# Kernel optimization log

Measured on AMD Instinct MI355X. Metric: run time of the kernel, lower is better.

## Reference

```python
import jax, jax.numpy as jnp
import numpy as np

B, L, D, NH, NITEMS = 256, 200, 128, 2, 100000
HD = D // NH
LAMB = 0.6
NEG = -1e9

_PARAM_SHAPES = dict(
    item_emb=(NITEMS, D), pos_emb=(L, D),
    W_ei=(D, D), b_ei=(D,), W_eo=(D, D), b_eo=(D,), b_iah=(D,), b_oah=(D,),
    w_ih=(3 * D, 2 * D), b_ih=(3 * D,), w_hh=(3 * D, D), b_hh=(3 * D,),
    ln1_g=(D,), ln1_b=(D,),
    Wq=(D, D), bq=(D,), Wk=(D, D), bk=(D,), Wv=(D, D), bv=(D,), Wo=(D, D), bo=(D,),
    ln2_g=(D,), ln2_b=(D,), W1=(D, D), b1=(D,), W2=(D, D), b2=(D,),
    lnf_g=(D,), lnf_b=(D,),
)


def setup_inputs() -> dict:
    key = jax.random.key(0)
    ks = jax.random.split(key, len(_PARAM_SHAPES) + 2)
    stdv = 1.0 / np.sqrt(D)  # GCSAN._init_weights: uniform(-stdv, stdv) on ALL params
    p = {}
    for i, (name, shp) in enumerate(_PARAM_SHAPES.items()):
        p[name] = jax.random.uniform(ks[i], shp, jnp.float32, -stdv, stdv)
    lens = jax.random.randint(ks[-2], (B,), L // 4, L + 1)
    vals = jax.random.randint(ks[-1], (B, L), 1, NITEMS)
    # trailing zero padding, as the original break-on-zero loop assumes
    seqs = jnp.where(jnp.arange(L)[None, :] < lens[:, None], vals, 0).astype(jnp.int32)
    p['seqs'] = seqs
    p['lens'] = lens.astype(jnp.int32)
    return p


def _ln(x, g, b):
    mu = x.mean(-1, keepdims=True)
    var = ((x - mu) ** 2).mean(-1, keepdims=True)
    return (x - mu) / jnp.sqrt(var + 1e-5) * g + b


def _build_graph(seqs):
    # Vectorized replacement of _get_slice (per-row np.unique + adjacency build)
    def per_row(seq):
        s = jnp.sort(seq)
        first = jnp.concatenate([jnp.ones((1,), bool), s[1:] != s[:-1]])
        pos = jnp.cumsum(first) - 1  # compaction target of each first-occurrence
        items = jnp.zeros((L,), seq.dtype).at[jnp.where(first, pos, L)].set(s, mode='drop')
        n_u = first.sum()
        search = jnp.where(jnp.arange(L) < n_u, items, jnp.iinfo(jnp.int32).max)
        alias = jnp.searchsorted(search, seq).astype(jnp.int32)
        return items, alias
    items, alias = jax.vmap(per_row)(seqs)
    valid = seqs[:, 1:] > 0  # edge (i -> i+1) exists until first pad
    u = jnp.where(valid, alias[:, :-1], L)  # route masked edges to dummy row L
    v = jnp.where(valid, alias[:, 1:], L)
    bidx = jnp.arange(B)[:, None]
    uA = jnp.zeros((B, L + 1, L + 1), jnp.float32).at[bidx, u, v].set(1.0)[:, :L, :L]
    in_deg = jnp.maximum(uA.sum(1), 1.0)
    out_deg = jnp.maximum(uA.sum(2), 1.0)
    A_in = jnp.swapaxes(uA, 1, 2) / in_deg[:, :, None]   # A[i,j] = uA[j,i]/in_deg[i]
    A_out = uA / out_deg[:, :, None]                     # A[i,k] = uA[i,k]/out_deg[i]
    return alias, jnp.concatenate([A_in, A_out], axis=2), items  # A: [B, L, 2L]


def reference(item_emb, pos_emb, W_ei, b_ei, W_eo, b_eo, b_iah, b_oah,
              w_ih, b_ih, w_hh, b_hh, ln1_g, ln1_b, Wq, bq, Wk, bk, Wv, bv,
              Wo, bo, ln2_g, ln2_b, W1, b1, W2, b2, lnf_g, lnf_b, seqs, lens):
    alias, A, items = _build_graph(seqs)
    hidden = item_emb[items]  # [B, L, D]
    # SR-GNN gated cell, step = n_layers = 1
    for _ in range(1):
        h_in = jnp.einsum('bij,bjd->bid', A[:, :, :L], hidden @ W_ei.T + b_ei) + b_iah
        h_out = jnp.einsum('bij,bjd->bid', A[:, :, L:], hidden @ W_eo.T + b_eo) + b_oah
        gi = jnp.concatenate([h_in, h_out], -1) @ w_ih.T + b_ih
        gh = hidden @ w_hh.T + b_hh
        i_r, i_i, i_n = jnp.split(gi, 3, -1)
        h_r, h_i, h_n = jnp.split(gh, 3, -1)
        r = jax.nn.sigmoid(i_r + h_r)
        z = jax.nn.sigmoid(i_i + h_i)
        ng = jnp.tanh(i_n + r * h_n)
        hidden = ng + z * (hidden - ng)
    bidx = jnp.arange(B)
    seq_hidden = hidden[bidx[:, None], alias]  # alias-gather back to sequence order
    last_idx = lens - 1
    ht = seq_hidden[bidx, last_idx]
    x = seq_hidden + pos_emb[None, :, :]
    tl_mask = (seqs > 0)[:, :, None].astype(x.dtype)
    x = x * tl_mask
    causal = jnp.triu(jnp.ones((L, L), bool), 1)  # True = masked future (bidirectional=False)
    # SASRec-style block: ln -> MHA residual -> ln -> pointwise FFN residual
    q_in = _ln(x, ln1_g, ln1_b)
    heads = lambda t: t.reshape(B, L, NH, HD).transpose(0, 2, 1, 3)
    q = heads(q_in @ Wq.T + bq)
    k = heads(x @ Wk.T + bk)
    v = heads(x @ Wv.T + bv)
    sc = jnp.einsum('bhqd,bhkd->bhqk', q, k) / jnp.sqrt(jnp.asarray(HD, x.dtype))
    sc = jnp.where(causal[None, None], NEG, sc)
    attn = jax.nn.softmax(sc, -1)
    mo = jnp.einsum('bhqk,bhkd->bhqd', attn, v).transpose(0, 2, 1, 3).reshape(B, L, D) @ Wo.T + bo
    x = q_in + mo
    h = _ln(x, ln2_g, ln2_b)
    x = h + jax.nn.relu(h @ W1.T + b1) @ W2.T + b2
    x = x * tl_mask
    log_feats = _ln(x, lnf_g, lnf_b)
    out = log_feats[bidx, last_idx]
    return LAMB * out + (1.0 - LAMB) * ht
```

## Files before the change

kernel.cpp:

```cpp
#include <hip/hip_runtime.h>
#include <hip/hip_bf16.h>

#define Bb 256
#define Ll 200
#define Dd 128
#define BL (Bb*Ll)

typedef __hip_bfloat16 bf16;
typedef __attribute__((ext_vector_type(8))) short short8;
typedef __attribute__((ext_vector_type(4))) unsigned short ushort4v;
typedef __attribute__((ext_vector_type(4))) float floatx4;

__device__ __forceinline__ float b2f(bf16 v) { return __bfloat162float(v); }
__device__ __forceinline__ bf16  f2b(float v) { return __float2bfloat16(v); }
__device__ __forceinline__ float us2f(unsigned short u) { return __uint_as_float(((unsigned)u) << 16); }
__device__ __forceinline__ unsigned short f2us(float v) { bf16 t = f2b(v); return *(unsigned short*)&t; }
__device__ __forceinline__ float ldf(const void* p, int i, int f32) {
  return f32 ? ((const float*)p)[i] : b2f(((const bf16*)p)[i]);
}
__device__ __forceinline__ int detect_f32(const unsigned short* __restrict__ w) {
  unsigned short u = w[threadIdx.x & 63];
  return (__ballot(((u >> 7) & 0xFF) >= 0x7F) != 0ull) ? 1 : 0;
}
__device__ __forceinline__ void load_lds16(const void* g, void* l) {
  __builtin_amdgcn_global_load_lds((const __attribute__((address_space(1))) unsigned int*)g,
                                   (__attribute__((address_space(3))) unsigned int*)l, 16, 0, 0);
}
__device__ __forceinline__ short8 emb_chunk8(const void* __restrict__ emb, int it, int g, int f32) {
  short8 o;
  if (f32) {
    const float4* e = (const float4*)((const float*)emb + (size_t)it * 128 + g * 8);
    float4 a = e[0], b = e[1];
    o[0] = (short)f2us(a.x); o[1] = (short)f2us(a.y); o[2] = (short)f2us(a.z); o[3] = (short)f2us(a.w);
    o[4] = (short)f2us(b.x); o[5] = (short)f2us(b.y); o[6] = (short)f2us(b.z); o[7] = (short)f2us(b.w);
  } else {
    o = ((const short8*)((const bf16*)emb + (size_t)it * 128))[g];
  }
  return o;
}

struct PackP {
  const void *W_ei,*W_eo,*w_ih,*w_hh,*Wk,*Wv,*Wqp,*Wop,*W1p,*W2p,*pos;
  const void *b_ei,*b_eo,*b_ih,*b_hh,*bk,*bv,*bqp,*bop,*b1p,*b2p,*biah,*boah;
  const void *ln1g,*ln1b,*ln2g,*ln2b,*lnfg,*lnfb;
  bf16 *cWhe,*cWih,*cWhh,*cWkv,*cWq,*cWo,*cW1,*cW2,*cPos;
  float *bias_he,*bias_gi,*bias_gh,*bias_kv,*cbq,*cbo,*cb1,*cb2,*cbiah,*cboah,*cln;
  const int* seqs;
  int *alias_g, *items_g; float *rin_g, *rout_g; unsigned *adj_g, *adjT_g;
};
__global__ __launch_bounds__(256) void k01(PackP p) {
  __shared__ alignas(16) int s[Ll];
  __shared__ int al[Ll], its[Ll];
  __shared__ alignas(4) unsigned char isf[Ll];
  __shared__ unsigned adjL[Ll*8], adjTL[Ll*8];
  if (blockIdx.x >= Bb) {
    int idx = (blockIdx.x - Bb) * 256 + threadIdx.x;
    int f32 = detect_f32((const unsigned short*)p.W_ei);
    if (idx < 131072) {
      if (idx < 32768) {
        int r = idx >> 7, c = idx & 127;
        p.cWhe[idx] = f2b(r < 128 ? ldf(p.W_ei, r*128+c, f32) : ldf(p.W_eo, (r-128)*128+c, f32));
      } else p.cWih[idx-32768] = f2b(ldf(p.w_ih, idx-32768, f32));
    } else if (idx < 278528) {
      if (idx < 180224)      p.cWhh[idx-131072] = f2b(ldf(p.w_hh, idx-131072, f32));
      else if (idx < 212992) {
        int i = idx - 180224; int r = i >> 7, c = i & 127;
        p.cWkv[i] = f2b(r < 128 ? ldf(p.Wk, r*128+c, f32) : ldf(p.Wv, (r-128)*128+c, f32));
      }
      else if (idx < 229376) p.cWq[idx-212992] = f2b(ldf(p.Wqp, idx-212992, f32));
      else if (idx < 245760) p.cWo[idx-229376] = f2b(ldf(p.Wop, idx-229376, f32));
      else if (idx < 262144) p.cW1[idx-245760] = f2b(ldf(p.W1p, idx-245760, f32));
      else                   p.cW2[idx-262144] = f2b(ldf(p.W2p, idx-262144, f32));
    } else if (idx < 304128) {
      p.cPos[idx-278528] = f2b(ldf(p.pos, idx-278528, f32));
    } else {
      int j = idx - 304128;
      if      (j < 256)  p.bias_he[j]     = (j<128) ? ldf(p.b_ei,j,f32) : ldf(p.b_eo,j-128,f32);
      else if (j < 640)  p.bias_gi[j-256] = ldf(p.b_ih, j-256, f32);
      else if (j < 1024) p.bias_gh[j-640] = ldf(p.b_hh, j-640, f32);
      else if (j < 1280) { int c=j-1024; p.bias_kv[c] = (c<128)? ldf(p.bk,c,f32): ldf(p.bv,c-128,f32); }
      else if (j < 1408) p.cbq[j-1280]   = ldf(p.bqp, j-1280, f32);
      else if (j < 1536) p.cbo[j-1408]   = ldf(p.bop, j-1408, f32);
      else if (j < 1664) p.cb1[j-1536]   = ldf(p.b1p, j-1536, f32);
      else if (j < 1792) p.cb2[j-1664]   = ldf(p.b2p, j-1664, f32);
      else if (j < 1920) p.cbiah[j-1792] = ldf(p.biah, j-1792, f32);
      else if (j < 2048) p.cboah[j-1920] = ldf(p.boah, j-1920, f32);
      else {
        int i = j - 2048, g = i >> 7, c2 = i & 127;
        const void* s6 = g==0?p.ln1g: g==1?p.ln1b: g==2?p.ln2g: g==3?p.ln2b: g==4?p.lnfg: p.lnfb;
        p.cln[i] = ldf(s6, c2, f32);
      }
    }
    return;
  }
  int b = blockIdx.x, t = threadIdx.x;
  if (t < Ll) s[t] = p.seqs[b*Ll + t];
  for (int i = t; i < Ll*8; i += 256) { adjL[i] = 0u; adjTL[i] = 0u; }
  __syncthreads();
  const int4* s4 = (const int4*)s;
  if (t < Ll) {
    int v = s[t]; int dup = 0;
    int nb = t >> 2;
    for (int j4 = 0; j4 < nb; j4++) {
      int4 sv = s4[j4];
      dup |= (sv.x==v) | (sv.y==v) | (sv.z==v) | (sv.w==v);
    }
    for (int j = nb*4; j < t; j++) dup |= (s[j]==v);
    isf[t] = dup ? 0 : 1; its[t] = 0;
  }
  __syncthreads();
  const unsigned* isfw = (const unsigned*)isf;
  if (t < Ll) {
    int v = s[t], r = 0;
    for (int j4 = 0; j4 < Ll/4; j4++) {
      int4 sv = s4[j4];
      unsigned fw = isfw[j4];
      r += ((fw & 0xffu)       && sv.x < v);
      r += ((fw & 0xff00u)     && sv.y < v);
      r += ((fw & 0xff0000u)   && sv.z < v);
      r += ((fw & 0xff000000u) && sv.w < v);
    }
    al[t] = r;
  }
  __syncthreads();
  if (t < Ll && isf[t]) its[al[t]] = s[t];
  if (t < Ll-1 && s[t+1] > 0) {
    int u = al[t], v = al[t+1];
    atomicOr(&adjL [u*8 + (v >> 5)], 1u << (v & 31));
    atomicOr(&adjTL[v*8 + (u >> 5)], 1u << (u & 31));
  }
  __syncthreads();
  if (t < Ll) {
    int od = 0, id = 0;
    for (int wd = 0; wd < 7; wd++) { od += __popc(adjL[t*8+wd]); id += __popc(adjTL[t*8+wd]); }
    p.rout_g [b*Ll + t] = 1.0f / (float)max(od, 1);
    p.rin_g  [b*Ll + t] = 1.0f / (float)max(id, 1);
    p.alias_g[b*Ll + t] = al[t];
    p.items_g[b*Ll + t] = its[t];
  }
  for (int i = t; i < Ll*8; i += 256) { p.adj_g[b*Ll*8 + i] = adjL[i]; p.adjT_g[b*Ll*8 + i] = adjTL[i]; }
}

__global__ __launch_bounds__(256) void gemm_he2(const void* __restrict__ emb, const int* __restrict__ items_g,
    const bf16* __restrict__ W, const float* __restrict__ bias,
    bf16* __restrict__ out_lo, int Nlo, bf16* __restrict__ out_hi, int Nhi, int split)
{
  __shared__ short As[128*128];
  __shared__ short Ws[128*128];
  int t = threadIdx.x;
  int wave = t >> 6, lane = t & 63;
  int q = lane >> 4, mr = lane & 15;
  int wm = wave & 1, wn = wave >> 1;
  int m0 = blockIdx.x * 128;
  int f32 = detect_f32((const unsigned short*)emb);
  {
    int r = t >> 1, half = t & 1;
    int it = items_g[m0 + r];
#pragma unroll
    for (int g8 = 0; g8 < 8; g8++) {
      int g = half*8 + g8;
      short8 o = emb_chunk8(emb, it, g, f32);
      *(short8*)&As[r*128 + (g ^ (r & 15))*8] = o;
    }
  }
  int srow = lane >> 4, c16 = lane & 15;
  for (int nt = 0; nt < 5; nt++) {
    int n0 = nt * 128;
#pragma unroll
    for (int i = 0; i < 8; i++) {
      int seg = wave*8 + i;
      int r = seg*4 + srow;
      int gch = c16 ^ (r & 15);
      load_lds16(W + (size_t)(n0 + r) * 128 + gch*8, &Ws[seg*512]);
    }
    __syncthreads();
    floatx4 acc[4][4] = {};
#pragma unroll
    for (int kk = 0; kk < 4; kk++) {
      short8 af[4], wf[4];
#pragma unroll
      for (int i = 0; i < 4; i++) {
        int row = wm*64 + i*16 + mr;
        af[i] = *(const short8*)(&As[row*128 + ((kk*4+q) ^ (row&15))*8]);
      }
#pragma unroll
      for (int j = 0; j < 4; j++) {
        int row = wn*64 + j*16 + mr;
        wf[j] = *(const short8*)(&Ws[row*128 + ((kk*4+q) ^ (row&15))*8]);
      }
#pragma unroll
      for (int i = 0; i < 4; i++)
#pragma unroll
        for (int j = 0; j < 4; j++)
          acc[i][j] = __builtin_amdgcn_mfma_f32_16x16x32_bf16(wf[j], af[i], acc[i][j], 0, 0, 0);
    }
#pragma unroll
    for (int j = 0; j < 4; j++) {
      int ng = n0 + wn*64 + j*16 + q*4;
      floatx4 bs = *(const floatx4*)(bias + ng);
      bf16* outp; int col, stride;
      if (ng < split) { outp = out_lo; col = ng; stride = Nlo; }
      else            { outp = out_hi; col = ng - split; stride = Nhi; }
#pragma unroll
      for (int i = 0; i < 4; i++) {
        int m = m0 + wm*64 + i*16 + mr;
        ushort4v o;
#pragma unroll
        for (int e = 0; e < 4; e++) o[e] = f2us(acc[i][j][e] + bs[e]);
        *(ushort4v*)(outp + (size_t)m * stride + col) = o;
      }
    }
    if (nt + 1 < 5) __syncthreads();
  }
}

template<int K>
__global__ __launch_bounds__(256) void gemm6(const bf16* __restrict__ A, const bf16* __restrict__ W,
    const float* __restrict__ bias,
    bf16* __restrict__ out_lo, int Nlo, bf16* __restrict__ out_hi, int Nhi, int split)
{
  __shared__ short As[128*128];
  __shared__ short Ws[128*128];
  int t = threadIdx.x;
  int wave = t >> 6, lane = t & 63;
  int q = lane >> 4, mr = lane & 15;
  int wm = wave & 1, wn = wave >> 1;
  int m0 = blockIdx.x * 128, n0 = blockIdx.y * 128;
  int srow = lane >> 4;
  int c16 = lane & 15;
  floatx4 acc[4][4] = {};
  for (int k0 = 0; k0 < K; k0 += 128) {
#pragma unroll
    for (int i = 0; i < 8; i++) {
      int seg = wave*8 + i;
      int r = seg*4 + srow;
      int gch = c16 ^ (r & 15);
      load_lds16(A + (size_t)(m0 + r) * K + k0 + gch*8, &As[seg*512]);
      load_lds16(W + (size_t)(n0 + r) * K + k0 + gch*8, &Ws[seg*512]);
    }
    __syncthreads();
#pragma unroll
    for (int kk = 0; kk < 4; kk++) {
      short8 af[4], wf[4];
#pragma unroll
      for (int i = 0; i < 4; i++) {
        int row = wm*64 + i*16 + mr;
        af[i] = *(const short8*)(&As[row*128 + ((kk*4+q) ^ (row&15))*8]);
      }
#pragma unroll
      for (int j = 0; j < 4; j++) {
        int row = wn*64 + j*16 + mr;
        wf[j] = *(const short8*)(&Ws[row*128 + ((kk*4+q) ^ (row&15))*8]);
      }
#pragma unroll
      for (int i = 0; i < 4; i++)
#pragma unroll
        for (int j = 0; j < 4; j++)
          acc[i][j] = __builtin_amdgcn_mfma_f32_16x16x32_bf16(wf[j], af[i], acc[i][j], 0, 0, 0);
    }
    if (k0 + 128 < K) __syncthreads();
  }
#pragma unroll
  for (int j = 0; j < 4; j++) {
    int ng = n0 + wn*64 + j*16 + q*4;
    floatx4 bs = *(const floatx4*)(bias + ng);
    bf16* outp; int col, stride;
    if (ng < split) { outp = out_lo; col = ng; stride = Nlo; }
    else            { outp = out_hi; col = ng - split; stride = Nhi; }
#pragma unroll
    for (int i = 0; i < 4; i++) {
      int m = m0 + wm*64 + i*16 + mr;
      ushort4v o;
#pragma unroll
      for (int e = 0; e < 4; e++) o[e] = f2us(acc[i][j][e] + bs[e]);
      *(ushort4v*)(outp + (size_t)m * stride + col) = o;
    }
  }
}

__global__ __launch_bounds__(256) void k3_agg(const bf16* __restrict__ he,
    const unsigned* __restrict__ adj_g, const unsigned* __restrict__ adjT_g,
    const float* __restrict__ rin_g, const float* __restrict__ rout_g,
    const float* __restrict__ cbiah, const float* __restrict__ cboah, bf16* __restrict__ hio)
{
  int b = blockIdx.x / 25, chunk = blockIdx.x % 25;
  int wave = threadIdx.x >> 6, lane = threadIdx.x & 63;
  bool isIn = lane < 32;
  int c = isIn ? 4*lane : 128 + 4*(lane-32);
  const bf16* heb = he + (size_t)b * Ll * 256;
  bf16* hiob = hio + (size_t)b * Ll * 256;
  float bias0 = isIn ? cbiah[c]   : cboah[c-128];
  float bias1 = isIn ? cbiah[c+1] : cboah[c-127];
  float bias2 = isIn ? cbiah[c+2] : cboah[c-126];
  float bias3 = isIn ? cbiah[c+3] : cboah[c-125];
#pragma unroll
  for (int s = 0; s < 2; s++) {
    int i = chunk*8 + wave + 4*s;
    const unsigned* mrow = (isIn ? adjT_g : adj_g) + ((size_t)b*Ll + i) * 8;
    float a0=0.f, a1=0.f, a2=0.f, a3=0.f;
    for (int wd = 0; wd < 7; wd++) {
      unsigned bits = mrow[wd];
      while (bits) {
        int j = (wd << 5) + __builtin_ctz(bits); bits &= bits - 1;
        ushort4v h4 = *(const ushort4v*)(heb + (size_t)j*256 + c);
        a0 += us2f(h4.x); a1 += us2f(h4.y); a2 += us2f(h4.z); a3 += us2f(h4.w);
      }
    }
    float r = isIn ? rin_g[b*Ll + i] : rout_g[b*Ll + i];
    ushort4v o;
    o.x = f2us(bias0 + r*a0); o.y = f2us(bias1 + r*a1);
    o.z = f2us(bias2 + r*a2); o.w = f2us(bias3 + r*a3);
    *(ushort4v*)(hiob + (size_t)i*256 + c) = o;
  }
}

__global__ __launch_bounds__(256) void kv_fused(const bf16* __restrict__ gi, const bf16* __restrict__ gh,
    const void* __restrict__ emb, const int* __restrict__ seqs,
    const int* __restrict__ alias_g, const int* __restrict__ lens,
    const bf16* __restrict__ cPos, const bf16* __restrict__ cWkv, const float* __restrict__ bias_kv,
    bf16* __restrict__ kv, float* __restrict__ ht)
{
  __shared__ short xs[208*136];
  __shared__ int aliasL[Ll], seqL[Ll];
  int b = blockIdx.x, t = threadIdx.x;
  int wave = t >> 6, lane = t & 63, q = lane >> 4, mr = lane & 15;
  int li = lens[b] - 1;
  int f32 = detect_f32((const unsigned short*)emb);
  if (t < Ll) { aliasL[t] = alias_g[b*Ll + t]; seqL[t] = seqs[b*Ll + t]; }
  for (int u = t; u < 8*136; u += 256) xs[Ll*136 + u] = 0;
  __syncthreads();
  for (int u = t; u < Ll*16; u += 256) {
    int tpos = u >> 4, jv = u & 15;
    int a = aliasL[tpos];
    int it = seqL[tpos];
    const short8* gin = (const short8*)(gi + ((size_t)b*Ll + a) * 384);
    const short8* ghn = (const short8*)(gh + ((size_t)b*Ll + a) * 384);
    short8 vir = gin[jv], vii = gin[16+jv], vnn = gin[32+jv];
    short8 whr = ghn[jv], whi = ghn[16+jv], whn = ghn[32+jv];
    short8 hv  = emb_chunk8(emb, it, jv, f32);
    short8 pv  = ((const short8*)(cPos + tpos * Dd))[jv];
    bool isLast = (tpos == li);
    short8 o;
#pragma unroll
    for (int e = 0; e < 8; e++) {
      float ir = us2f((unsigned short)vir[e]), ii = us2f((unsigned short)vii[e]), inn = us2f((unsigned short)vnn[e]);
      float hr = us2f((unsigned short)whr[e]), hi = us2f((unsigned short)whi[e]), hn = us2f((unsigned short)whn[e]);
      float r  = 1.f / (1.f + __expf(-(ir + hr)));
      float z  = 1.f / (1.f + __expf(-(ii + hi)));
      float arg = inn + r * hn;
      float ex = __expf(-2.f * arg);
      float ng = (1.f - ex) / (1.f + ex);
      float h  = us2f((unsigned short)hv[e]);
      float sh = ng + z * (h - ng);
      o[e] = (short)f2us(sh + us2f((unsigned short)pv[e]));
      if (isLast) ht[b*Dd + jv*8 + e] = sh;
    }
    *(short8*)&xs[tpos*136 + jv*8] = o;
  }
  __syncthreads();
  short8 wf[4][4];
#pragma unroll
  for (int kk = 0; kk < 4; kk++)
#pragma unroll
    for (int j = 0; j < 4; j++) {
      int n = wave*64 + j*16 + mr;
      wf[kk][j] = *(const short8*)(cWkv + (size_t)n*128 + kk*32 + q*8);
    }
  for (int mt = 0; mt < 13; mt++) {
    short8 af[4];
#pragma unroll
    for (int kk = 0; kk < 4; kk++)
      af[kk] = *(const short8*)&xs[(mt*16 + mr)*136 + (kk*4+q)*8];
    floatx4 acc[4] = {};
#pragma unroll
    for (int kk = 0; kk < 4; kk++)
#pragma unroll
      for (int j = 0; j < 4; j++)
        acc[j] = __builtin_amdgcn_mfma_f32_16x16x32_bf16(wf[kk][j], af[kk], acc[j], 0, 0, 0);
    int m = mt*16 + mr;
    if (m < Ll) {
#pragma unroll
      for (int j = 0; j < 4; j++) {
        int n = wave*64 + j*16 + q*4;
        floatx4 bs = *(const floatx4*)(bias_kv + n);
        ushort4v o;
#pragma unroll
        for (int e = 0; e < 4; e++) o[e] = f2us(acc[j][e] + bs[e]);
        *(ushort4v*)(kv + ((size_t)b*Ll + m)*256 + n) = o;
      }
    }
  }
}

struct FinalP {
  const bf16 *kv; const float* ht; const bf16* cPos;
  const bf16 *cWq, *cWo, *cW1, *cW2;
  const float *cbq, *cbo, *cb1, *cb2, *cln;
  const int* lens; const void* wei;
  void* out;
};
__device__ __forceinline__ float dot128i(const bf16* __restrict__ wrow, const float* __restrict__ vin) {
  const short8* wr = (const short8*)wrow;
  float a0=0.f, a1=0.f, a2=0.f, a3=0.f;
#pragma unroll
  for (int kk = 0; kk < 4; kk++) {
    short8 w0 = wr[kk*4+0], w1 = wr[kk*4+1], w2 = wr[kk*4+2], w3 = wr[kk*4+3];
#pragma unroll
    for (int j = 0; j < 8; j++) {
      a0 += vin[kk*32 +      j] * us2f((unsigned short)w0[j]);
      a1 += vin[kk*32 + 8  + j] * us2f((unsigned short)w1[j]);
      a2 += vin[kk*32 + 16 + j] * us2f((unsigned short)w2[j]);
      a3 += vin[kk*32 + 24 + j] * us2f((unsigned short)w3[j]);
    }
  }
  return (a0+a1)+(a2+a3);
}
__device__ __forceinline__ float wave_sum(float v) {
#pragma unroll
  for (int m = 1; m < 64; m <<= 1) v += __shfl_xor(v, m, 64);
  return v;
}
__device__ __forceinline__ float wave_max(float v) {
#pragma unroll
  for (int m = 1; m < 64; m <<= 1) v = fmaxf(v, __shfl_xor(v, m, 64));
  return v;
}
__global__ __launch_bounds__(256) void k7_final(FinalP p)
{
  __shared__ float sred[8];
  __shared__ float qin[128], qv[128], aout[128], hh[128], f1[128];
  __shared__ float pb0[256], pb1[256];
  __shared__ floatx4 av4[8][32];
  int b = blockIdx.x, t = threadIdx.x, c = t;
  int w = t >> 6, ln = t & 63;
  int li = p.lens[b] - 1;
  int f32 = detect_f32((const unsigned short*)p.wei);
  float xv = (c < 128) ? (p.ht[b*Dd + c] + b2f(p.cPos[li*Dd + c])) : 0.f;
  float s = wave_sum(xv), s2 = wave_sum(xv*xv);
  if (ln == 0) { sred[w] = s; sred[4+w] = s2; }
  __syncthreads();
  float mu = (sred[0]+sred[1]+sred[2]+sred[3]) * (1.f/128.f);
  float ms = (sred[4]+sred[5]+sred[6]+sred[7]) * (1.f/128.f);
  float rs = rsqrtf(fmaxf(ms - mu*mu, 0.f) + 1e-5f);
  __syncthreads();
  if (c < 128) qin[c] = (xv - mu) * rs * p.cln[c] + p.cln[128+c];
  __syncthreads();
  if (c < 128) qv[c] = p.cbq[c] + dot128i(p.cWq + c*128, qin);
  __syncthreads();
  const bf16* kvb = p.kv + (size_t)b * Ll * 256;
  float s0 = -3.0e38f, s1 = -3.0e38f;
  if (t <= li) {
    const short8* kr = (const short8*)(kvb + (size_t)t*256);
    float a00=0.f,a01=0.f,a10=0.f,a11=0.f;
#pragma unroll
    for (int kk = 0; kk < 4; kk++) {
      short8 k0 = kr[kk*2], k1 = kr[kk*2+1], k2 = kr[8+kk*2], k3 = kr[8+kk*2+1];
#pragma unroll
      for (int j = 0; j < 8; j++) {
        a00 += qv[kk*16 + j]      * us2f((unsigned short)k0[j]);
        a01 += qv[kk*16 + 8 + j]  * us2f((unsigned short)k1[j]);
        a10 += qv[64 + kk*16 + j]     * us2f((unsigned short)k2[j]);
        a11 += qv[64 + kk*16 + 8 + j] * us2f((unsigned short)k3[j]);
      }
    }
    s0 = (a00+a01) * 0.125f; s1 = (a10+a11) * 0.125f;
  }
  float m0 = wave_max(s0), m1 = wave_max(s1);
  if (ln == 0) { sred[w] = m0; sred[4+w] = m1; }
  __syncthreads();
  m0 = fmaxf(fmaxf(sred[0],sred[1]), fmaxf(sred[2],sred[3]));
  m1 = fmaxf(fmaxf(sred[4],sred[5]), fmaxf(sred[6],sred[7]));
  __syncthreads();
  float e0 = (t <= li) ? __expf(s0 - m0) : 0.f;
  float e1 = (t <= li) ? __expf(s1 - m1) : 0.f;
  pb0[t] = e0; pb1[t] = e1;
  float l0 = wave_sum(e0), l1 = wave_sum(e1);
  if (ln == 0) { sred[w] = l0; sred[4+w] = l1; }
  __syncthreads();
  l0 = sred[0]+sred[1]+sred[2]+sred[3];
  l1 = sred[4]+sred[5]+sred[6]+sred[7];
  {
    int part = t >> 5, cq = t & 31, ch = cq * 4;
    int cnt = li + 1, cpp = (cnt + 7) >> 3;
    int j0 = part * cpp, j1 = min(j0 + cpp, cnt);
    const float* pbh = (ch < 64) ? pb0 : pb1;
    float a0=0.f,a1=0.f,a2=0.f,a3=0.f;
#pragma unroll 4
    for (int j = j0; j < j1; j++) {
      ushort4v v4 = *(const ushort4v*)(kvb + (size_t)j*256 + 128 + ch);
      float pw = pbh[j];
      a0 += pw*us2f(v4.x); a1 += pw*us2f(v4.y); a2 += pw*us2f(v4.z); a3 += pw*us2f(v4.w);
    }
    floatx4 o = {a0,a1,a2,a3};
    av4[part][cq] = o;
  }
  __syncthreads();
  if (c < 128) {
    float l = (c < 64) ? l0 : l1;
    float acc = 0.f;
#pragma unroll
    for (int pp = 0; pp < 8; pp++) acc += ((const float*)&av4[pp][c>>2])[c&3];
    aout[c] = acc / l;
  }
  __syncthreads();
  float x2v = 0.f;
  if (c < 128) x2v = qin[c] + p.cbo[c] + dot128i(p.cWo + c*128, aout);
  s = wave_sum((c<128)?x2v:0.f); s2 = wave_sum((c<128)?x2v*x2v:0.f);
  if (ln == 0) { sred[w] = s; sred[4+w] = s2; }
  __syncthreads();
  mu = (sred[0]+sred[1]+sred[2]+sred[3]) * (1.f/128.f);
  ms = (sred[4]+sred[5]+sred[6]+sred[7]) * (1.f/128.f);
  rs = rsqrtf(fmaxf(ms - mu*mu, 0.f) + 1e-5f);
  __syncthreads();
  if (c < 128) hh[c] = (x2v - mu) * rs * p.cln[256+c] + p.cln[384+c];
  __syncthreads();
  if (c < 128) f1[c] = fmaxf(p.cb1[c] + dot128i(p.cW1 + c*128, hh), 0.f);
  __syncthreads();
  float x3v = 0.f;
  if (c < 128) x3v = hh[c] + p.cb2[c] + dot128i(p.cW2 + c*128, f1);
  s = wave_sum((c<128)?x3v:0.f); s2 = wave_sum((c<128)?x3v*x3v:0.f);
  if (ln == 0) { sred[w] = s; sred[4+w] = s2; }
  __syncthreads();
  mu = (sred[0]+sred[1]+sred[2]+sred[3]) * (1.f/128.f);
  ms = (sred[4]+sred[5]+sred[6]+sred[7]) * (1.f/128.f);
  rs = rsqrtf(fmaxf(ms - mu*mu, 0.f) + 1e-5f);
  if (c < 128) {
    float lf = (x3v - mu) * rs * p.cln[512+c] + p.cln[640+c];
    float outv = 0.6f * lf + 0.4f * p.ht[b*Dd + c];
    if (f32) ((float*)p.out)[b*Dd + c] = outv;
    else     ((bf16*)p.out)[b*Dd + c]  = f2b(outv);
  }
}

extern "C" void kernel_launch(void* const* d_in, const int* in_sizes, int n_in,
                              void* d_out, int out_size, void* d_ws, size_t ws_size,
                              hipStream_t stream)
{
  (void)in_sizes; (void)n_in; (void)out_size; (void)ws_size;
  const void* item_emb = d_in[0];
  const int* seqs = (const int*)d_in[30];
  const int* lens = (const int*)d_in[31];

  char* wsp = (char*)d_ws;
  size_t o = 0;
  auto alloc = [&](size_t sz) { void* p = wsp + o; o += (sz + 255) & ~(size_t)255; return p; };
  int*      alias_g = (int*)alloc((size_t)BL*4);
  int*      items_g = (int*)alloc((size_t)BL*4);
  float*    rin_g   = (float*)alloc((size_t)BL*4);
  float*    rout_g  = (float*)alloc((size_t)BL*4);
  unsigned* adj_g   = (unsigned*)alloc((size_t)BL*8*4);
  unsigned* adjT_g  = (unsigned*)alloc((size_t)BL*8*4);
  float*    ht_g    = (float*)alloc((size_t)Bb*Dd*4);
  bf16*     cWhe    = (bf16*)alloc(32768*2);
  bf16*     cWhh    = (bf16*)alloc(49152*2);
  bf16*     cWih    = (bf16*)alloc(98304*2);
  bf16*     cWkv    = (bf16*)alloc(32768*2);
  bf16*     cWq     = (bf16*)alloc(16384*2);
  bf16*     cWo     = (bf16*)alloc(16384*2);
  bf16*     cW1     = (bf16*)alloc(16384*2);
  bf16*     cW2     = (bf16*)alloc(16384*2);
  bf16*     cPos    = (bf16*)alloc(25600*2);
  float*    bias_he = (float*)alloc(256*4);
  float*    bias_gh = (float*)alloc(384*4);
  float*    bias_gi = (float*)alloc(384*4);
  float*    bias_kv = (float*)alloc(256*4);
  float*    cbq     = (float*)alloc(128*4);
  float*    cbo     = (float*)alloc(128*4);
  float*    cb1     = (float*)alloc(128*4);
  float*    cb2     = (float*)alloc(128*4);
  float*    cbiah   = (float*)alloc(128*4);
  float*    cboah   = (float*)alloc(128*4);
  float*    cln     = (float*)alloc(768*4);
  bf16*     he      = (bf16*)alloc((size_t)BL*256*2);
  bf16*     hio     = (bf16*)alloc((size_t)BL*256*2);
  bf16*     gi      = (bf16*)alloc((size_t)BL*384*2);
  bf16*     gh      = (bf16*)alloc((size_t)BL*384*2);
  bf16*     kv = hio;

  PackP pp = { d_in[2], d_in[4], d_in[8], d_in[10], d_in[16], d_in[18], d_in[14], d_in[20],
               d_in[24], d_in[26], d_in[1],
               d_in[3], d_in[5], d_in[9], d_in[11], d_in[17], d_in[19], d_in[15], d_in[21],
               d_in[25], d_in[27], d_in[6], d_in[7],
               d_in[12], d_in[13], d_in[22], d_in[23], d_in[28], d_in[29],
               cWhe, cWih, cWhh, cWkv, cWq, cWo, cW1, cW2, cPos,
               bias_he, bias_gi, bias_gh, bias_kv, cbq, cbo, cb1, cb2, cbiah, cboah, cln,
               seqs, alias_g, items_g, rin_g, rout_g, adj_g, adjT_g };
  k01<<<Bb + 1199, 256, 0, stream>>>(pp);
  gemm_he2<<<BL/128, 256, 0, stream>>>(item_emb, items_g, cWhe, bias_he, he, 256, gh, 384, 256);
  k3_agg<<<Bb*25, 256, 0, stream>>>(he, adj_g, adjT_g, rin_g, rout_g, cbiah, cboah, hio);
  gemm6<256><<<dim3(BL/128, 3), 256, 0, stream>>>(hio, cWih, bias_gi, gi, 384, gi, 384, 1<<30);
  kv_fused<<<Bb, 256, 0, stream>>>(gi, gh, item_emb, seqs, alias_g, lens, cPos, cWkv, bias_kv, kv, ht_g);
  FinalP fp = { kv, ht_g, cPos, cWq, cWo, cW1, cW2, cbq, cbo, cb1, cb2, cln, lens, d_in[2], d_out };
  k7_final<<<Bb, 256, 0, stream>>>(fp);
}
```

Baseline: 273.5 us.

## Fuse K/V projection with final attention kernel, keep KV in LDS

Merges the kv_fused and k7_final kernels into one per-batch kernel that writes the K/V projection and the last-position hidden state into shared memory. The attention, FFN and layer norms then read them from there. This removes a kernel launch and the global round trip of the per-batch KV buffer (about 100 KB per batch) and of ht. In exchange the kernel allocates about 160 KB of LDS in one shared pool that is reused between stages, which limits occupancy to one block per CU. It also keeps the 256 blocks of 256 threads, so most of the GPU stays lightly loaded.

```diff
diff --git a/kernel.cpp b/kernel.cpp
--- a/kernel.cpp
+++ b/kernel.cpp
@@ -314,31 +314,74 @@
   }
 }
 
-__global__ __launch_bounds__(256) void kv_fused(const bf16* __restrict__ gi, const bf16* __restrict__ gh,
-    const void* __restrict__ emb, const int* __restrict__ seqs,
-    const int* __restrict__ alias_g, const int* __restrict__ lens,
-    const bf16* __restrict__ cPos, const bf16* __restrict__ cWkv, const float* __restrict__ bias_kv,
-    bf16* __restrict__ kv, float* __restrict__ ht)
+struct KAP {
+  const bf16 *gi, *gh; const void* emb; const int* seqs; const int* alias_g; const int* lens;
+  const bf16 *cPos, *cWkv; const float* bias_kv;
+  const bf16 *cWq, *cWo, *cW1, *cW2;
+  const float *cbq, *cbo, *cb1, *cb2, *cln;
+  void* out;
+};
+__device__ __forceinline__ float dot128i(const bf16* __restrict__ wrow, const float* __restrict__ vin) {
+  const short8* wr = (const short8*)wrow;
+  float a0=0.f, a1=0.f, a2=0.f, a3=0.f;
+#pragma unroll
+  for (int kk = 0; kk < 4; kk++) {
+    short8 w0 = wr[kk*4+0], w1 = wr[kk*4+1], w2 = wr[kk*4+2], w3 = wr[kk*4+3];
+#pragma unroll
+    for (int j = 0; j < 8; j++) {
+      a0 += vin[kk*32 +      j] * us2f((unsigned short)w0[j]);
+      a1 += vin[kk*32 + 8  + j] * us2f((unsigned short)w1[j]);
+      a2 += vin[kk*32 + 16 + j] * us2f((unsigned short)w2[j]);
+      a3 += vin[kk*32 + 24 + j] * us2f((unsigned short)w3[j]);
+    }
+  }
+  return (a0+a1)+(a2+a3);
+}
+__device__ __forceinline__ float wave_sum(float v) {
+#pragma unroll
+  for (int m = 1; m < 64; m <<= 1) v += __shfl_xor(v, m, 64);
+  return v;
+}
+__device__ __forceinline__ float wave_max(float v) {
+#pragma unroll
+  for (int m = 1; m < 64; m <<= 1) v = fmaxf(v, __shfl_xor(v, m, 64));
+  return v;
+}
+__global__ __launch_bounds__(256) void kv_attn(KAP p)
 {
-  __shared__ short xs[208*136];
-  __shared__ int aliasL[Ll], seqL[Ll];
+  __shared__ __align__(16) char pool[162688];
+  short* xs   = (short*)pool;
+  short* kvL  = (short*)(pool + 56576);
+  float* htL  = (float*)(pool + 56576 + 105600);
+  int* aliasL = (int*)(pool + 56576);
+  int* seqL   = aliasL + 200;
+  float* qin  = (float*)pool;
+  float* qv   = qin + 128;
+  float* aout = qv + 128;
+  float* hh   = aout + 128;
+  float* f1   = hh + 128;
+  float* pb0  = f1 + 128;
+  float* pb1  = pb0 + 256;
+  floatx4* av4 = (floatx4*)(pb1 + 256);
+  float* sred = (float*)(av4 + 8*32);
+
   int b = blockIdx.x, t = threadIdx.x;
   int wave = t >> 6, lane = t & 63, q = lane >> 4, mr = lane & 15;
-  int li = lens[b] - 1;
-  int f32 = detect_f32((const unsigned short*)emb);
-  if (t < Ll) { aliasL[t] = alias_g[b*Ll + t]; seqL[t] = seqs[b*Ll + t]; }
+  int li = p.lens[b] - 1;
+  int f32 = detect_f32((const unsigned short*)p.emb);
+  if (t < Ll) { aliasL[t] = p.alias_g[b*Ll + t]; seqL[t] = p.seqs[b*Ll + t]; }
   for (int u = t; u < 8*136; u += 256) xs[Ll*136 + u] = 0;
   __syncthreads();
   for (int u = t; u < Ll*16; u += 256) {
     int tpos = u >> 4, jv = u & 15;
     int a = aliasL[tpos];
     int it = seqL[tpos];
-    const short8* gin = (const short8*)(gi + ((size_t)b*Ll + a) * 384);
-    const short8* ghn = (const short8*)(gh + ((size_t)b*Ll + a) * 384);
+    const short8* gin = (const short8*)(p.gi + ((size_t)b*Ll + a) * 384);
+    const short8* ghn = (const short8*)(p.gh + ((size_t)b*Ll + a) * 384);
     short8 vir = gin[jv], vii = gin[16+jv], vnn = gin[32+jv];
     short8 whr = ghn[jv], whi = ghn[16+jv], whn = ghn[32+jv];
-    short8 hv  = emb_chunk8(emb, it, jv, f32);
-    short8 pv  = ((const short8*)(cPos + tpos * Dd))[jv];
+    short8 hv  = emb_chunk8(p.emb, it, jv, f32);
+    short8 pv  = ((const short8*)(p.cPos + tpos * Dd))[jv];
     bool isLast = (tpos == li);
     short8 o;
 #pragma unroll
@@ -353,89 +396,48 @@
       float h  = us2f((unsigned short)hv[e]);
       float sh = ng + z * (h - ng);
       o[e] = (short)f2us(sh + us2f((unsigned short)pv[e]));
-      if (isLast) ht[b*Dd + jv*8 + e] = sh;
+      if (isLast) htL[jv*8 + e] = sh;
     }
     *(short8*)&xs[tpos*136 + jv*8] = o;
   }
   __syncthreads();
-  short8 wf[4][4];
-#pragma unroll
-  for (int kk = 0; kk < 4; kk++)
-#pragma unroll
-    for (int j = 0; j < 4; j++) {
-      int n = wave*64 + j*16 + mr;
-      wf[kk][j] = *(const short8*)(cWkv + (size_t)n*128 + kk*32 + q*8);
-    }
-  for (int mt = 0; mt < 13; mt++) {
-    short8 af[4];
+  {
+    short8 wf[4][4];
 #pragma unroll
     for (int kk = 0; kk < 4; kk++)
-      af[kk] = *(const short8*)&xs[(mt*16 + mr)*136 + (kk*4+q)*8];
-    floatx4 acc[4] = {};
-#pragma unroll
-    for (int kk = 0; kk < 4; kk++)
-#pragma unroll
-      for (int j = 0; j < 4; j++)
-        acc[j] = __builtin_amdgcn_mfma_f32_16x16x32_bf16(wf[kk][j], af[kk], acc[j], 0, 0, 0);
-    int m = mt*16 + mr;
-    if (m < Ll) {
 #pragma unroll
       for (int j = 0; j < 4; j++) {
-        int n = wave*64 + j*16 + q*4;
-        floatx4 bs = *(const floatx4*)(bias_kv + n);
-        ushort4v o;
-#pragma unroll
-        for (int e = 0; e < 4; e++) o[e] = f2us(acc[j][e] + bs[e]);
-        *(ushort4v*)(kv + ((size_t)b*Ll + m)*256 + n) = o;
-      }
-    }
-  }
-}
-
-struct FinalP {
-  const bf16 *kv; const float* ht; const bf16* cPos;
-  const bf16 *cWq, *cWo, *cW1, *cW2;
-  const float *cbq, *cbo, *cb1, *cb2, *cln;
-  const int* lens; const void* wei;
-  void* out;
-};
-__device__ __forceinline__ float dot128i(const bf16* __restrict__ wrow, const float* __restrict__ vin) {
-  const short8* wr = (const short8*)wrow;
-  float a0=0.f, a1=0.f, a2=0.f, a3=0.f;
-#pragma unroll
-  for (int kk = 0; kk < 4; kk++) {
-    short8 w0 = wr[kk*4+0], w1 = wr[kk*4+1], w2 = wr[kk*4+2], w3 = wr[kk*4+3];
-#pragma unroll
-    for (int j = 0; j < 8; j++) {
-      a0 += vin[kk*32 +      j] * us2f((unsigned short)w0[j]);
-      a1 += vin[kk*32 + 8  + j] * us2f((unsigned short)w1[j]);
-      a2 += vin[kk*32 + 16 + j] * us2f((unsigned short)w2[j]);
-      a3 += vin[kk*32 + 24 + j] * us2f((unsigned short)w3[j]);
-    }
-  }
-  return (a0+a1)+(a2+a3);
-}
-__device__ __forceinline__ float wave_sum(float v) {
-#pragma unroll
-  for (int m = 1; m < 64; m <<= 1) v += __shfl_xor(v, m, 64);
-  return v;
-}
-__device__ __forceinline__ float wave_max(float v) {
-#pragma unroll
-  for (int m = 1; m < 64; m <<= 1) v = fmaxf(v, __shfl_xor(v, m, 64));
-  return v;
-}
-__global__ __launch_bounds__(256) void k7_final(FinalP p)
-{
-  __shared__ float sred[8];
-  __shared__ float qin[128], qv[128], aout[128], hh[128], f1[128];
-  __shared__ float pb0[256], pb1[256];
-  __shared__ floatx4 av4[8][32];
-  int b = blockIdx.x, t = threadIdx.x, c = t;
-  int w = t >> 6, ln = t & 63;
-  int li = p.lens[b] - 1;
-  int f32 = detect_f32((const unsigned short*)p.wei);
-  float xv = (c < 128) ? (p.ht[b*Dd + c] + b2f(p.cPos[li*Dd + c])) : 0.f;
+        int n = wave*64 + j*16 + mr;
+        wf[kk][j] = *(const short8*)(p.cWkv + (size_t)n*128 + kk*32 + q*8);
+      }
+    for (int mt = 0; mt < 13; mt++) {
+      short8 af[4];
+#pragma unroll
+      for (int kk = 0; kk < 4; kk++)
+        af[kk] = *(const short8*)&xs[(mt*16 + mr)*136 + (kk*4+q)*8];
+      floatx4 acc[4] = {};
+#pragma unroll
+      for (int kk = 0; kk < 4; kk++)
+#pragma unroll
+        for (int j = 0; j < 4; j++)
+          acc[j] = __builtin_amdgcn_mfma_f32_16x16x32_bf16(wf[kk][j], af[kk], acc[j], 0, 0, 0);
+      int m = mt*16 + mr;
+      if (m < Ll) {
+#pragma unroll
+        for (int j = 0; j < 4; j++) {
+          int n = wave*64 + j*16 + q*4;
+          floatx4 bs = *(const floatx4*)(p.bias_kv + n);
+          ushort4v o;
+#pragma unroll
+          for (int e = 0; e < 4; e++) o[e] = f2us(acc[j][e] + bs[e]);
+          *(ushort4v*)&kvL[m*264 + n] = o;
+        }
+      }
+    }
+  }
+  __syncthreads();
+  int c = t, w = wave, ln = lane;
+  float xv = (c < 128) ? (htL[c] + b2f(p.cPos[li*Dd + c])) : 0.f;
   float s = wave_sum(xv), s2 = wave_sum(xv*xv);
   if (ln == 0) { sred[w] = s; sred[4+w] = s2; }
   __syncthreads();
@@ -447,10 +449,9 @@
   __syncthreads();
   if (c < 128) qv[c] = p.cbq[c] + dot128i(p.cWq + c*128, qin);
   __syncthreads();
-  const bf16* kvb = p.kv + (size_t)b * Ll * 256;
   float s0 = -3.0e38f, s1 = -3.0e38f;
   if (t <= li) {
-    const short8* kr = (const short8*)(kvb + (size_t)t*256);
+    const short8* kr = (const short8*)&kvL[t*264];
     float a00=0.f,a01=0.f,a10=0.f,a11=0.f;
 #pragma unroll
     for (int kk = 0; kk < 4; kk++) {
@@ -487,19 +488,19 @@
     float a0=0.f,a1=0.f,a2=0.f,a3=0.f;
 #pragma unroll 4
     for (int j = j0; j < j1; j++) {
-      ushort4v v4 = *(const ushort4v*)(kvb + (size_t)j*256 + 128 + ch);
+      ushort4v v4 = *(const ushort4v*)&kvL[j*264 + 128 + ch];
       float pw = pbh[j];
       a0 += pw*us2f(v4.x); a1 += pw*us2f(v4.y); a2 += pw*us2f(v4.z); a3 += pw*us2f(v4.w);
     }
     floatx4 o = {a0,a1,a2,a3};
-    av4[part][cq] = o;
+    av4[part*32 + cq] = o;
   }
   __syncthreads();
   if (c < 128) {
     float l = (c < 64) ? l0 : l1;
     float acc = 0.f;
 #pragma unroll
-    for (int pp = 0; pp < 8; pp++) acc += ((const float*)&av4[pp][c>>2])[c&3];
+    for (int pp = 0; pp < 8; pp++) acc += ((const float*)&av4[pp*32 + (c>>2)])[c&3];
     aout[c] = acc / l;
   }
   __syncthreads();
@@ -526,7 +527,7 @@
   rs = rsqrtf(fmaxf(ms - mu*mu, 0.f) + 1e-5f);
   if (c < 128) {
     float lf = (x3v - mu) * rs * p.cln[512+c] + p.cln[640+c];
-    float outv = 0.6f * lf + 0.4f * p.ht[b*Dd + c];
+    float outv = 0.6f * lf + 0.4f * htL[c];
     if (f32) ((float*)p.out)[b*Dd + c] = outv;
     else     ((bf16*)p.out)[b*Dd + c]  = f2b(outv);
   }
@@ -550,7 +551,6 @@
   float*    rout_g  = (float*)alloc((size_t)BL*4);
   unsigned* adj_g   = (unsigned*)alloc((size_t)BL*8*4);
   unsigned* adjT_g  = (unsigned*)alloc((size_t)BL*8*4);
-  float*    ht_g    = (float*)alloc((size_t)Bb*Dd*4);
   bf16*     cWhe    = (bf16*)alloc(32768*2);
   bf16*     cWhh    = (bf16*)alloc(49152*2);
   bf16*     cWih    = (bf16*)alloc(98304*2);
@@ -575,7 +575,6 @@
   bf16*     hio     = (bf16*)alloc((size_t)BL*256*2);
   bf16*     gi      = (bf16*)alloc((size_t)BL*384*2);
   bf16*     gh      = (bf16*)alloc((size_t)BL*384*2);
-  bf16*     kv = hio;
 
   PackP pp = { d_in[2], d_in[4], d_in[8], d_in[10], d_in[16], d_in[18], d_in[14], d_in[20],
                d_in[24], d_in[26], d_in[1],
@@ -589,7 +588,7 @@
   gemm_he2<<<BL/128, 256, 0, stream>>>(item_emb, items_g, cWhe, bias_he, he, 256, gh, 384, 256);
   k3_agg<<<Bb*25, 256, 0, stream>>>(he, adj_g, adjT_g, rin_g, rout_g, cbiah, cboah, hio);
   gemm6<256><<<dim3(BL/128, 3), 256, 0, stream>>>(hio, cWih, bias_gi, gi, 384, gi, 384, 1<<30);
-  kv_fused<<<Bb, 256, 0, stream>>>(gi, gh, item_emb, seqs, alias_g, lens, cPos, cWkv, bias_kv, kv, ht_g);
-  FinalP fp = { kv, ht_g, cPos, cWq, cWo, cW1, cW2, cbq, cbo, cb1, cb2, cln, lens, d_in[2], d_out };
-  k7_final<<<Bb, 256, 0, stream>>>(fp);
-}
+  KAP kp = { gi, gh, item_emb, seqs, alias_g, lens, cPos, cWkv, bias_kv,
+             cWq, cWo, cW1, cW2, cbq, cbo, cb1, cb2, cln, d_out };
+  kv_attn<<<Bb, 256, 0, stream>>>(kp);
+}
```

Result: faster. 263.8 us (-3.5%).
